# Kernel optimization log

Measured on AMD Instinct MI355X. Metric: run time of the kernel, lower is better.

The kernel has to match this reference:

```python
import jax, jax.numpy as jnp
import numpy as np

D_MODEL = 1024
NUM_HEADS = 16
D_HEAD = D_MODEL // NUM_HEADS
THETA = 10000.0


def setup_inputs() -> dict:
    key = jax.random.key(0)
    ks = jax.random.split(key, 5)
    B, S = 2, 2048
    std = np.sqrt(2.0 / (D_MODEL + D_MODEL))
    return {
        "x": jax.random.normal(ks[0], (B, S, D_MODEL), dtype=jnp.float32),
        "token_positions": jnp.arange(S, dtype=jnp.int32),
        "wq": jax.random.normal(ks[1], (D_MODEL, D_MODEL), dtype=jnp.float32) * std,
        "wk": jax.random.normal(ks[2], (D_MODEL, D_MODEL), dtype=jnp.float32) * std,
        "wv": jax.random.normal(ks[3], (D_MODEL, D_MODEL), dtype=jnp.float32) * std,
        "wo": jax.random.normal(ks[4], (D_MODEL, D_MODEL), dtype=jnp.float32) * std,
    }


def _rope(x, token_positions):
    # x: [B, H, S, D_HEAD]; token_positions: [S]
    freq_idx = jnp.arange(0, D_HEAD, 2, dtype=jnp.float32)
    inv_freq = THETA ** (-freq_idx / D_HEAD)                      # [D_HEAD/2]
    angles = token_positions.astype(jnp.float32)[:, None] * inv_freq  # [S, D_HEAD/2]
    cos = jnp.cos(angles)[None, None, :, :]
    sin = jnp.sin(angles)[None, None, :, :]
    x_even = x[..., 0::2]
    x_odd = x[..., 1::2]
    rot_even = x_even * cos - x_odd * sin
    rot_odd = x_even * sin + x_odd * cos
    # interleave pairs back: [..., pairs, 2] -> [..., D_HEAD]
    return jnp.stack((rot_even, rot_odd), axis=-1).reshape(x.shape)


def reference(x, token_positions, wq, wk, wv, wo):
    B, S, _ = x.shape
    def proj(w):
        y = jnp.einsum('bsi,oi->bso', x, w)
        return y.reshape(B, S, NUM_HEADS, D_HEAD).transpose(0, 2, 1, 3)  # [B,H,S,Dh]
    q = _rope(proj(wq), token_positions)
    k = _rope(proj(wk), token_positions)
    v = proj(wv)
    scores = jnp.einsum('bhqd,bhkd->bhqk', q, k) / jnp.sqrt(jnp.float32(D_HEAD))
    causal = jnp.tril(jnp.ones((S, S), dtype=bool))
    scores = jnp.where(causal, scores, -jnp.inf)
    probs = jax.nn.softmax(scores, axis=-1)
    attn = jnp.einsum('bhqk,bhkd->bhqd', probs, v)
    attn = attn.transpose(0, 2, 1, 3).reshape(B, S, D_MODEL)
    return jnp.einsum('bsi,oi->bso', attn, wo)
```

## Files before the change

### kernel.cpp

```cpp
#include <hip/hip_runtime.h>
#include <math.h>

#define D_MODEL 1024
#define NUM_HEADS 16
#define D_HEAD 64
#define SEQ 2048
#define BATCH 2

typedef __attribute__((ext_vector_type(8))) short short8;
typedef __attribute__((ext_vector_type(4))) short short4v;
typedef __attribute__((ext_vector_type(4))) float float4v;
typedef __attribute__((ext_vector_type(2))) unsigned int uint2v;

__device__ __forceinline__ short f2bf(float f) {
    unsigned u = __float_as_uint(f);
    u += 0x7FFFu + ((u >> 16) & 1u);
    return (short)(u >> 16);
}

__device__ __forceinline__ float fexp2(float x) {
    return __builtin_amdgcn_exp2f(x);
}

__global__ __launch_bounds__(256) void cvt_bf16_kernel(
    const float* __restrict__ x,  const float* __restrict__ wq,
    const float* __restrict__ wk, const float* __restrict__ wv,
    const float* __restrict__ wo, const int* __restrict__ pos,
    short* __restrict__ xb,  short* __restrict__ wqb,
    short* __restrict__ wkb, short* __restrict__ wvb,
    short* __restrict__ wob,
    float* __restrict__ costab, float* __restrict__ sintab)
{
    const int a = blockIdx.y;
    if (a == 5) {
        const int idx = blockIdx.x * 256 + threadIdx.x;
        if (idx < SEQ * 32) {
            const int s = idx >> 5, fi = idx & 31;
            const float p = (float)pos[s];
            const float inv_freq = exp2f((float)fi * -0.4152410118609203f);
            float sn, cs;
            sincosf(p * inv_freq, &sn, &cs);
            costab[idx] = cs;
            sintab[idx] = sn;
        }
        return;
    }
    const float* src = (a == 0) ? x : (a == 1) ? wq : (a == 2) ? wk : (a == 3) ? wv : wo;
    short* dst = (a == 0) ? xb : (a == 1) ? wqb : (a == 2) ? wkb : (a == 3) ? wvb : wob;
    const int n = (a == 0) ? (BATCH * SEQ * D_MODEL) : (D_MODEL * D_MODEL);
    const int i = (blockIdx.x * 256 + threadIdx.x) * 8;
    if (i >= n) return;
    const float4 v0 = *(const float4*)(src + i);
    const float4 v1 = *(const float4*)(src + i + 4);
    short8 r;
    r[0] = f2bf(v0.x); r[1] = f2bf(v0.y); r[2] = f2bf(v0.z); r[3] = f2bf(v0.w);
    r[4] = f2bf(v1.x); r[5] = f2bf(v1.y); r[6] = f2bf(v1.z); r[7] = f2bf(v1.w);
    *(short8*)(dst + i) = r;
}

__device__ __forceinline__ void gemm_core_db(
    const short* __restrict__ a, const short* __restrict__ b,
    short* smem, int m0, int n0, float4v acc[4][4])
{
    const int tid = threadIdx.x;
    const int lane = tid & 63;
    const int l15 = lane & 15, quad = lane >> 4;
    const int wave = tid >> 6;
    const int mw = (wave & 1) * 64, nw = (wave >> 1) * 64;
    const int srow = tid >> 2;
    const int scol = (tid & 3) * 8;
    const int ssw = (((tid & 3) ^ ((srow >> 1) & 3))) * 8;
    const int xsw = (l15 >> 1) & 3;

    const short* ag = a + (size_t)(m0 + srow) * D_MODEL + scol;
    const short* bg = b + (size_t)(n0 + srow) * D_MODEL + scol;

    short* bufA[2] = { smem,        smem + 8192 };
    short* bufB[2] = { smem + 4096, smem + 12288 };

    short8 ga0 = *(const short8*)(ag);
    short8 ga1 = *(const short8*)(ag + (size_t)64 * D_MODEL);
    short8 gb0 = *(const short8*)(bg);
    short8 gb1 = *(const short8*)(bg + (size_t)64 * D_MODEL);
    *(short8*)&bufA[0][srow * 32 + ssw]        = ga0;
    *(short8*)&bufA[0][(64 + srow) * 32 + ssw] = ga1;
    *(short8*)&bufB[0][srow * 32 + ssw]        = gb0;
    *(short8*)&bufB[0][(64 + srow) * 32 + ssw] = gb1;
    ga0 = *(const short8*)(ag + 32);
    ga1 = *(const short8*)(ag + 32 + (size_t)64 * D_MODEL);
    gb0 = *(const short8*)(bg + 32);
    gb1 = *(const short8*)(bg + 32 + (size_t)64 * D_MODEL);

    for (int k = 0; k < 32; k++) {
        __syncthreads();
        if (k + 1 < 32) {
            short* bA = bufA[(k + 1) & 1];
            short* bB = bufB[(k + 1) & 1];
            *(short8*)&bA[srow * 32 + ssw]        = ga0;
            *(short8*)&bA[(64 + srow) * 32 + ssw] = ga1;
            *(short8*)&bB[srow * 32 + ssw]        = gb0;
            *(short8*)&bB[(64 + srow) * 32 + ssw] = gb1;
        }
        if (k + 2 < 32) {
            const int off = (k + 2) * 32;
            ga0 = *(const short8*)(ag + off);
            ga1 = *(const short8*)(ag + off + (size_t)64 * D_MODEL);
            gb0 = *(const short8*)(bg + off);
            gb1 = *(const short8*)(bg + off + (size_t)64 * D_MODEL);
        }
        const short* lA = bufA[k & 1];
        const short* lB = bufB[k & 1];
        short8 af[4], bf[4];
        #pragma unroll
        for (int i = 0; i < 4; i++)
            af[i] = *(const short8*)&lA[(mw + i * 16 + l15) * 32 + (quad ^ xsw) * 8];
        #pragma unroll
        for (int i = 0; i < 4; i++)
            bf[i] = *(const short8*)&lB[(nw + i * 16 + l15) * 32 + (quad ^ xsw) * 8];
        #pragma unroll
        for (int mi = 0; mi < 4; mi++)
            #pragma unroll
            for (int ni = 0; ni < 4; ni++)
                acc[mi][ni] = __builtin_amdgcn_mfma_f32_16x16x32_bf16(
                    af[mi], bf[ni], acc[mi][ni], 0, 0, 0);
    }
}

__global__ __launch_bounds__(256) void qkv_mfma_kernel(
    const short* __restrict__ xb, const short* __restrict__ wqb,
    const short* __restrict__ wkb, const short* __restrict__ wvb,
    const float* __restrict__ costab, const float* __restrict__ sintab,
    short* __restrict__ Qb, short* __restrict__ Kb, short* __restrict__ Vt)
{
    __shared__ __align__(16) short smem[128 * 136];

    const int z = blockIdx.x >> 8;
    const int bid = blockIdx.x & 255;
    const int m0 = (bid & 31) * 128;
    const int n0 = (bid >> 5) * 128;
    const short* w = (z == 0) ? wqb : (z == 1) ? wkb : wvb;

    float4v acc[4][4];
    #pragma unroll
    for (int i = 0; i < 4; i++)
        #pragma unroll
        for (int j = 0; j < 4; j++)
            acc[i][j] = (float4v){0.f, 0.f, 0.f, 0.f};

    gemm_core_db(xb, w, smem, m0, n0, acc);

    const int tid = threadIdx.x;
    const int lane = tid & 63;
    const int l15 = lane & 15, quad = lane >> 4;
    const int wave = tid >> 6;
    const int mw = (wave & 1) * 64, nw = (wave >> 1) * 64;
    const int s_base = m0 & (SEQ - 1);
    const int bb = m0 >> 11;

    __syncthreads();

    if (z == 2) {
        #pragma unroll
        for (int ni = 0; ni < 4; ni++) {
            #pragma unroll
            for (int mi = 0; mi < 4; mi++) {
                #pragma unroll
                for (int r = 0; r < 4; r++)
                    smem[(nw + ni * 16 + l15) * 136 + mw + mi * 16 + quad * 4 + r] =
                        f2bf(acc[mi][ni][r]);
            }
        }
        __syncthreads();
        #pragma unroll
        for (int it = 0; it < 8; it++) {
            const int nloc = it * 16 + (tid >> 4);
            const int mloc = (tid & 15) * 8;
            const short8 val = *(const short8*)&smem[nloc * 136 + mloc];
            const int n = n0 + nloc;
            const int h = n >> 6, d = n & 63;
            *(short8*)(Vt + ((size_t)(bb * NUM_HEADS + h) * D_HEAD + d) * SEQ +
                       s_base + mloc) = val;
        }
    } else {
        short* dst = (z == 0) ? Qb : Kb;
        const float qs = (z == 0) ? 0.18033688011112042f : 1.0f;
        #pragma unroll
        for (int ni = 0; ni < 4; ni++) {
            const int n = n0 + nw + ni * 16 + l15;
            const int d = n & 63;
            const int fi = d >> 1;
            #pragma unroll
            for (int mi = 0; mi < 4; mi++) {
                #pragma unroll
                for (int r = 0; r < 4; r++) {
                    const int mloc = mw + mi * 16 + quad * 4 + r;
                    const int ti = ((s_base + mloc) << 5) + fi;
                    const float cs = costab[ti];
                    const float sn = sintab[ti];
                    const float val = acc[mi][ni][r];
                    const float partner = __shfl_xor(val, 1, 64);
                    const float res = (l15 & 1) ? fmaf(partner, sn, val * cs)
                                                : fmaf(val, cs, -partner * sn);
                    smem[mloc * 136 + nw + ni * 16 + l15] = f2bf(res * qs);
                }
            }
        }
        __syncthreads();
        #pragma unroll
        for (int it = 0; it < 8; it++) {
            const int ri = it * 32 + (tid >> 3);
            const int mloc = ri & 127;
            const int hh = ri >> 7;
            const int nloc = hh * 64 + (tid & 7) * 8;
            const short8 val = *(const short8*)&smem[mloc * 136 + nloc];
            const int n = n0 + nloc;
            const int h = n >> 6, d = n & 63;
            *(short8*)(dst + ((size_t)(bb * NUM_HEADS + h) * SEQ + s_base + mloc) *
                       D_HEAD + d) = val;
        }
    }
}

__global__ __launch_bounds__(256) void attn_mfma_kernel(
    const short* __restrict__ Qb, const short* __restrict__ Kb,
    const short* __restrict__ Vt, short* __restrict__ Ab)
{
    __shared__ __align__(16) short lK[64 * 72];
    __shared__ __align__(16) short lV[64 * 72];
    __shared__ __align__(16) short lP[4][16 * 72];

    const int tid = threadIdx.x;
    const int lane = tid & 63;
    const int wave = tid >> 6;
    const int l15 = lane & 15;
    const int quad = lane >> 4;

    const int bh = blockIdx.x & (BATCH * NUM_HEADS - 1);
    const int qt = (SEQ / 64 - 1) - (blockIdx.x >> 5);
    const int q0w = qt * 64 + wave * 16;
    const int qcmp = q0w + l15;

    const short* Kg = Kb + (size_t)bh * SEQ * D_HEAD;
    const short* Vg = Vt + (size_t)bh * D_HEAD * SEQ;

    const short* Qrow = Qb + ((size_t)bh * SEQ + q0w + l15) * D_HEAD;
    const short8 qf0 = *(const short8*)(Qrow + quad * 8);
    const short8 qf1 = *(const short8*)(Qrow + 32 + quad * 8);

    float4v o0 = {0.f, 0.f, 0.f, 0.f}, o1 = o0, o2 = o0, o3 = o0;
    float lpA = 0.f, lpB = 0.f;

    const int nt = qt + 1;
    const int srow = tid >> 2;
    const int c4  = tid & 3;
    const int sch = c4 * 8;
    const int w1off = srow * 72 + c4 * 16;

    short8 k0 = *(const short8*)(Kg + (size_t)srow * D_HEAD + sch);
    short8 k1 = *(const short8*)(Kg + (size_t)srow * D_HEAD + sch + 32);
    short8 v0 = *(const short8*)(Vg + (size_t)srow * SEQ + sch);
    short8 v1 = *(const short8*)(Vg + (size_t)srow * SEQ + sch + 32);

#define ATTN_TILE_COMPUTE(KT0, MASKED)                                        \
    {                                                                         \
        short* Pw = lP[wave];                                                 \
        _Pragma("unroll")                                                     \
        for (int g = 0; g < 4; g++) {                                         \
            float4v s = {0.f, 0.f, 0.f, 0.f};                                 \
            const short8 ka = *(const short8*)&lK[(g * 16 + l15) * 72 + quad * 16];     \
            s = __builtin_amdgcn_mfma_f32_16x16x32_bf16(ka, qf0, s, 0, 0, 0); \
            const short8 kb = *(const short8*)&lK[(g * 16 + l15) * 72 + quad * 16 + 8]; \
            s = __builtin_amdgcn_mfma_f32_16x16x32_bf16(kb, qf1, s, 0, 0, 0); \
            float e0, e1, e2, e3;                                             \
            if (MASKED) {                                                     \
                const int kbase = (KT0) + g * 16 + quad * 4;                  \
                e0 = (kbase + 0 <= qcmp) ? fexp2(s[0]) : 0.f;                 \
                e1 = (kbase + 1 <= qcmp) ? fexp2(s[1]) : 0.f;                 \
                e2 = (kbase + 2 <= qcmp) ? fexp2(s[2]) : 0.f;                 \
                e3 = (kbase + 3 <= qcmp) ? fexp2(s[3]) : 0.f;                 \
            } else {                                                          \
                e0 = fexp2(s[0]); e1 = fexp2(s[1]);                           \
                e2 = fexp2(s[2]); e3 = fexp2(s[3]);                           \
            }                                                                 \
            lpA += e0 + e2;                                                   \
            lpB += e1 + e3;                                                   \
            unsigned int pw0, pw1;                                            \
            asm("v_cvt_pk_bf16_f32 %0, %1, %2" : "=v"(pw0) : "v"(e0), "v"(e1)); \
            asm("v_cvt_pk_bf16_f32 %0, %1, %2" : "=v"(pw1) : "v"(e2), "v"(e3)); \
            uint2v pk; pk[0] = pw0; pk[1] = pw1;                              \
            *(uint2v*)&Pw[l15 * 72 + g * 16 + quad * 4] = pk;                 \
        }                                                                     \
        const short8 pa0 = *(const short8*)&lP[wave][l15 * 72 + quad * 8];    \
        const short8 pa1 = *(const short8*)&lP[wave][l15 * 72 + 32 + quad * 8]; \
        _Pragma("unroll")                                                     \
        for (int j = 0; j < 4; j++) {                                         \
            const short8 va = *(const short8*)&lV[(j * 16 + l15) * 72 + quad * 16];     \
            const short8 vb = *(const short8*)&lV[(j * 16 + l15) * 72 + quad * 16 + 8]; \
            float4v* oj = (j == 0) ? &o0 : (j == 1) ? &o1 : (j == 2) ? &o2 : &o3;       \
            *oj = __builtin_amdgcn_mfma_f32_16x16x32_bf16(pa0, va, *oj, 0, 0, 0);       \
            *oj = __builtin_amdgcn_mfma_f32_16x16x32_bf16(pa1, vb, *oj, 0, 0, 0);       \
        }                                                                     \
    }

    for (int t = 0; t < nt - 1; t++) {
        const int kt0 = t * 64;
        __syncthreads();
        *(short8*)&lK[w1off]     = k0;
        *(short8*)&lK[w1off + 8] = k1;
        *(short8*)&lV[w1off]     = v0;
        *(short8*)&lV[w1off + 8] = v1;
        __syncthreads();
        k0 = *(const short8*)(Kg + (size_t)(kt0 + 64 + srow) * D_HEAD + sch);
        k1 = *(const short8*)(Kg + (size_t)(kt0 + 64 + srow) * D_HEAD + sch + 32);
        v0 = *(const short8*)(Vg + (size_t)srow * SEQ + kt0 + 64 + sch);
        v1 = *(const short8*)(Vg + (size_t)srow * SEQ + kt0 + 64 + sch + 32);
        ATTN_TILE_COMPUTE(kt0, false)
    }
    {
        const int kt0 = (nt - 1) * 64;
        __syncthreads();
        *(short8*)&lK[w1off]     = k0;
        *(short8*)&lK[w1off + 8] = k1;
        *(short8*)&lV[w1off]     = v0;
        *(short8*)&lV[w1off + 8] = v1;
        __syncthreads();
        ATTN_TILE_COMPUTE(kt0, true)
    }
#undef ATTN_TILE_COMPUTE

    float lp = lpA + lpB;
    lp += __shfl_xor(lp, 16, 64);
    lp += __shfl_xor(lp, 32, 64);

    const int b = bh >> 4, h = bh & 15;
    short* Ap = Ab + ((size_t)(b * SEQ) + q0w + quad * 4) * D_MODEL + h * D_HEAD;
    #pragma unroll
    for (int r = 0; r < 4; r++) {
        const float inv = 1.0f / __shfl(lp, quad * 4 + r, 64);
        Ap[(size_t)r * D_MODEL + l15]      = f2bf(o0[r] * inv);
        Ap[(size_t)r * D_MODEL + 16 + l15] = f2bf(o1[r] * inv);
        Ap[(size_t)r * D_MODEL + 32 + l15] = f2bf(o2[r] * inv);
        Ap[(size_t)r * D_MODEL + 48 + l15] = f2bf(o3[r] * inv);
    }
}

__global__ __launch_bounds__(256) void out_mfma_kernel(
    const short* __restrict__ Ab, const short* __restrict__ wob,
    float* __restrict__ out)
{
    __shared__ __align__(16) short smem[2 * 8192];

    const int bid = blockIdx.x;
    const int m0 = (bid & 31) * 128;
    const int n0 = (bid >> 5) * 128;

    float4v acc[4][4];
    #pragma unroll
    for (int i = 0; i < 4; i++)
        #pragma unroll
        for (int j = 0; j < 4; j++)
            acc[i][j] = (float4v){0.f, 0.f, 0.f, 0.f};

    gemm_core_db(Ab, wob, smem, m0, n0, acc);

    const int tid = threadIdx.x;
    const int lane = tid & 63;
    const int l15 = lane & 15, quad = lane >> 4;
    const int wave = tid >> 6;
    const int mw = (wave & 1) * 64, nw = (wave >> 1) * 64;

    #pragma unroll
    for (int mi = 0; mi < 4; mi++) {
        #pragma unroll
        for (int r = 0; r < 4; r++) {
            const int m = m0 + mw + mi * 16 + quad * 4 + r;
            float* op = out + (size_t)m * D_MODEL + n0 + nw + l15;
            #pragma unroll
            for (int ni = 0; ni < 4; ni++)
                op[ni * 16] = acc[mi][ni][r];
        }
    }
}

extern "C" void kernel_launch(void* const* d_in, const int* in_sizes, int n_in,
                              void* d_out, int out_size, void* d_ws, size_t ws_size,
                              hipStream_t stream)
{
    const float* x  = (const float*)d_in[0];
    const int*  pos = (const int*)d_in[1];
    const float* wq = (const float*)d_in[2];
    const float* wk = (const float*)d_in[3];
    const float* wv = (const float*)d_in[4];
    const float* wo = (const float*)d_in[5];
    float* out = (float*)d_out;

    const size_t nx = (size_t)BATCH * SEQ * D_MODEL;
    const size_t nw = (size_t)D_MODEL * D_MODEL;
    short* xb  = (short*)d_ws;
    short* wqb = xb + nx;
    short* wkb = wqb + nw;
    short* wvb = wkb + nw;
    short* wob = wvb + nw;
    short* Qb  = wob + nw;
    short* Kb  = Qb + nx;
    short* Vt  = Kb + nx;
    short* Ab  = Vt + nx;
    float* costab = (float*)(Ab + nx);
    float* sintab = costab + SEQ * 32;

    dim3 blk(256);
    cvt_bf16_kernel<<<dim3(2048, 6), blk, 0, stream>>>(x, wq, wk, wv, wo, pos,
                                                       xb, wqb, wkb, wvb, wob,
                                                       costab, sintab);
    qkv_mfma_kernel<<<dim3(768), blk, 0, stream>>>(xb, wqb, wkb, wvb,
                                                   costab, sintab, Qb, Kb, Vt);
    attn_mfma_kernel<<<dim3(BATCH * NUM_HEADS * (SEQ / 64)), blk, 0, stream>>>(Qb, Kb, Vt, Ab);
    out_mfma_kernel<<<dim3(256), blk, 0, stream>>>(Ab, wob, out);
}
```

Baseline: 183.4 us.

## Load K/V fragments directly from global memory instead of staging in LDS

The attention kernel no longer stages K and V tiles in shared memory. Each wave now reads its MFMA operand fragments for every key tile straight from global memory into registers, which removes both block-wide barriers and the LDS writes and reads for K/V. In exchange, each of the four waves fetches the same K/V data separately, which quadruples global/L2 traffic. The register prefetch of the next tile is also gone, so load latency is exposed at the start of each tile unless occupancy hides it.

New measurement: 275.0 us. 1.5x slower.

```diff
diff --git a/kernel.cpp b/kernel.cpp
--- a/kernel.cpp
+++ b/kernel.cpp
@@ -225,8 +225,6 @@
     const short* __restrict__ Qb, const short* __restrict__ Kb,
     const short* __restrict__ Vt, short* __restrict__ Ab)
 {
-    __shared__ __align__(16) short lK[64 * 72];
-    __shared__ __align__(16) short lV[64 * 72];
     __shared__ __align__(16) short lP[4][16 * 72];
 
     const int tid = threadIdx.x;
@@ -251,26 +249,28 @@
     float lpA = 0.f, lpB = 0.f;
 
     const int nt = qt + 1;
-    const int srow = tid >> 2;
-    const int c4  = tid & 3;
-    const int sch = c4 * 8;
-    const int w1off = srow * 72 + c4 * 16;
-
-    short8 k0 = *(const short8*)(Kg + (size_t)srow * D_HEAD + sch);
-    short8 k1 = *(const short8*)(Kg + (size_t)srow * D_HEAD + sch + 32);
-    short8 v0 = *(const short8*)(Vg + (size_t)srow * SEQ + sch);
-    short8 v1 = *(const short8*)(Vg + (size_t)srow * SEQ + sch + 32);
-
-#define ATTN_TILE_COMPUTE(KT0, MASKED)                                        \
+    short* Pw = lP[wave];
+
+#define ATTN_TILE(KT0, MASKED)                                                \
     {                                                                         \
-        short* Pw = lP[wave];                                                 \
+        short8 ka[4], kb[4], va[4], vb[4];                                    \
+        _Pragma("unroll")                                                     \
+        for (int g = 0; g < 4; g++) {                                         \
+            const short* kr = Kg + (size_t)((KT0) + g * 16 + l15) * D_HEAD + quad * 8; \
+            ka[g] = *(const short8*)kr;                                       \
+            kb[g] = *(const short8*)(kr + 32);                                \
+        }                                                                     \
+        _Pragma("unroll")                                                     \
+        for (int j = 0; j < 4; j++) {                                         \
+            const short* vr = Vg + (size_t)(j * 16 + l15) * SEQ + (KT0) + quad * 8; \
+            va[j] = *(const short8*)vr;                                       \
+            vb[j] = *(const short8*)(vr + 32);                                \
+        }                                                                     \
         _Pragma("unroll")                                                     \
         for (int g = 0; g < 4; g++) {                                         \
             float4v s = {0.f, 0.f, 0.f, 0.f};                                 \
-            const short8 ka = *(const short8*)&lK[(g * 16 + l15) * 72 + quad * 16];     \
-            s = __builtin_amdgcn_mfma_f32_16x16x32_bf16(ka, qf0, s, 0, 0, 0); \
-            const short8 kb = *(const short8*)&lK[(g * 16 + l15) * 72 + quad * 16 + 8]; \
-            s = __builtin_amdgcn_mfma_f32_16x16x32_bf16(kb, qf1, s, 0, 0, 0); \
+            s = __builtin_amdgcn_mfma_f32_16x16x32_bf16(ka[g], qf0, s, 0, 0, 0); \
+            s = __builtin_amdgcn_mfma_f32_16x16x32_bf16(kb[g], qf1, s, 0, 0, 0); \
             float e0, e1, e2, e3;                                             \
             if (MASKED) {                                                     \
                 const int kbase = (KT0) + g * 16 + quad * 4;                  \
@@ -290,43 +290,23 @@
             uint2v pk; pk[0] = pw0; pk[1] = pw1;                              \
             *(uint2v*)&Pw[l15 * 72 + g * 16 + quad * 4] = pk;                 \
         }                                                                     \
-        const short8 pa0 = *(const short8*)&lP[wave][l15 * 72 + quad * 8];    \
-        const short8 pa1 = *(const short8*)&lP[wave][l15 * 72 + 32 + quad * 8]; \
-        _Pragma("unroll")                                                     \
-        for (int j = 0; j < 4; j++) {                                         \
-            const short8 va = *(const short8*)&lV[(j * 16 + l15) * 72 + quad * 16];     \
-            const short8 vb = *(const short8*)&lV[(j * 16 + l15) * 72 + quad * 16 + 8]; \
-            float4v* oj = (j == 0) ? &o0 : (j == 1) ? &o1 : (j == 2) ? &o2 : &o3;       \
-            *oj = __builtin_amdgcn_mfma_f32_16x16x32_bf16(pa0, va, *oj, 0, 0, 0);       \
-            *oj = __builtin_amdgcn_mfma_f32_16x16x32_bf16(pa1, vb, *oj, 0, 0, 0);       \
-        }                                                                     \
+        const short8 pa0 = *(const short8*)&Pw[l15 * 72 + quad * 8];          \
+        const short8 pa1 = *(const short8*)&Pw[l15 * 72 + 32 + quad * 8];     \
+        o0 = __builtin_amdgcn_mfma_f32_16x16x32_bf16(pa0, va[0], o0, 0, 0, 0); \
+        o0 = __builtin_amdgcn_mfma_f32_16x16x32_bf16(pa1, vb[0], o0, 0, 0, 0); \
+        o1 = __builtin_amdgcn_mfma_f32_16x16x32_bf16(pa0, va[1], o1, 0, 0, 0); \
+        o1 = __builtin_amdgcn_mfma_f32_16x16x32_bf16(pa1, vb[1], o1, 0, 0, 0); \
+        o2 = __builtin_amdgcn_mfma_f32_16x16x32_bf16(pa0, va[2], o2, 0, 0, 0); \
+        o2 = __builtin_amdgcn_mfma_f32_16x16x32_bf16(pa1, vb[2], o2, 0, 0, 0); \
+        o3 = __builtin_amdgcn_mfma_f32_16x16x32_bf16(pa0, va[3], o3, 0, 0, 0); \
+        o3 = __builtin_amdgcn_mfma_f32_16x16x32_bf16(pa1, vb[3], o3, 0, 0, 0); \
     }
 
     for (int t = 0; t < nt - 1; t++) {
-        const int kt0 = t * 64;
-        __syncthreads();
-        *(short8*)&lK[w1off]     = k0;
-        *(short8*)&lK[w1off + 8] = k1;
-        *(short8*)&lV[w1off]     = v0;
-        *(short8*)&lV[w1off + 8] = v1;
-        __syncthreads();
-        k0 = *(const short8*)(Kg + (size_t)(kt0 + 64 + srow) * D_HEAD + sch);
-        k1 = *(const short8*)(Kg + (size_t)(kt0 + 64 + srow) * D_HEAD + sch + 32);
-        v0 = *(const short8*)(Vg + (size_t)srow * SEQ + kt0 + 64 + sch);
-        v1 = *(const short8*)(Vg + (size_t)srow * SEQ + kt0 + 64 + sch + 32);
-        ATTN_TILE_COMPUTE(kt0, false)
-    }
-    {
-        const int kt0 = (nt - 1) * 64;
-        __syncthreads();
-        *(short8*)&lK[w1off]     = k0;
-        *(short8*)&lK[w1off + 8] = k1;
-        *(short8*)&lV[w1off]     = v0;
-        *(short8*)&lV[w1off + 8] = v1;
-        __syncthreads();
-        ATTN_TILE_COMPUTE(kt0, true)
-    }
-#undef ATTN_TILE_COMPUTE
+        ATTN_TILE(t * 64, false)
+    }
+    ATTN_TILE((nt - 1) * 64, true)
+#undef ATTN_TILE
 
     float lp = lpA + lpB;
     lp += __shfl_xor(lp, 16, 64);
```
